# Performance work log

Hardware: AMD Instinct MI355X
Metric: run time of the kernel (lower is better)

## Reference

```python
import jax, jax.numpy as jnp
import numpy as np
import math

B, N, C_IN = 16, 4096, 1024
D, M, K, H = 64, 16, 64, 4  # projected dim, n prototypes, topk, heads


def setup_inputs() -> dict:
    key = jax.random.key(0)
    ks = jax.random.split(key, 8)
    return {
        "image_features": jax.random.normal(ks[0], (B, N, C_IN), jnp.float32),
        "W_down": jax.random.normal(ks[1], (C_IN, D), jnp.float32) * 0.02,
        "b_down": jnp.zeros((D,), jnp.float32),
        "W_up": jax.random.normal(ks[2], (D, C_IN), jnp.float32) * 0.02,
        "b_up": jnp.zeros((C_IN,), jnp.float32),
        "m_queries": jax.random.normal(ks[3], (1, M, D), jnp.float32),
        "ln_w": jnp.ones((D,), jnp.float32),
        "ln_b": jnp.zeros((D,), jnp.float32),
        "in_proj_w": jax.random.normal(ks[4], (3 * D, D), jnp.float32) * 0.05,
        "in_proj_b": jnp.zeros((3 * D,), jnp.float32),
        "out_proj_w": jax.random.normal(ks[5], (D, D), jnp.float32) * 0.05,
        "out_proj_b": jnp.zeros((D,), jnp.float32),
        "gamma": jnp.asarray(0.1, jnp.float32),
    }


@jax.custom_vjp
def ste_topk_mask(logits):
    # TopkSTE.forward: one-hot mask of top-k along dim 1
    _, idx = jax.lax.top_k(logits, K)
    oh = jnp.zeros_like(logits).at[jnp.arange(logits.shape[0])[:, None], idx].set(1.0)
    return oh


def _ste_fwd(logits):
    return ste_topk_mask(logits), logits


def _ste_bwd(logits, g):
    # TopkSTE.backward: grad_output * softmax(logits)
    return (g * jax.nn.softmax(logits, axis=1),)


ste_topk_mask.defvjp(_ste_fwd, _ste_bwd)


def _layernorm(x, w, b, eps=1e-5):
    mu = x.mean(-1, keepdims=True)
    var = ((x - mu) ** 2).mean(-1, keepdims=True)
    return (x - mu) * jax.lax.rsqrt(var + eps) * w + b


def _mha(x, in_w, in_b, out_w, out_b):
    # nn.MultiheadAttention self-attention, batch_first; x: [B,S,D]
    b, s, d = x.shape
    dh = d // H
    qkv = x @ in_w.T + in_b  # [B,S,3D]
    q, k, v = jnp.split(qkv, 3, axis=-1)
    split = lambda t: t.reshape(b, s, H, dh).transpose(0, 2, 1, 3)  # [B,H,S,dh]
    q, k, v = split(q), split(k), split(v)
    scores = jnp.einsum('bhqd,bhkd->bhqk', q, k) * (1.0 / math.sqrt(dh))
    attn = jax.nn.softmax(scores, axis=-1)
    o = jnp.einsum('bhqk,bhkd->bhqd', attn, v)
    o = o.transpose(0, 2, 1, 3).reshape(b, s, d)
    return o @ out_w.T + out_b


def reference(image_features, W_down, b_down, W_up, b_up, m_queries,
              ln_w, ln_b, in_proj_w, in_proj_b, out_proj_w, out_proj_b, gamma):
    identity = image_features
    act = jax.nn.gelu(image_features @ W_down + b_down)  # [B,N,D]; dropout = eval no-op

    # cosine similarity against prototypes -> max over prototypes
    nf = act / (jnp.linalg.norm(act, axis=-1, keepdims=True) + 1e-12)
    q0 = m_queries[0]
    nq = q0 / (jnp.linalg.norm(q0, axis=-1, keepdims=True) + 1e-12)
    scores = jnp.einsum('bnd,md->bnm', nf, nq).max(-1)  # [B,N]

    _ = ste_topk_mask(scores)  # mask only used to derive indices in original
    # torch mask.nonzero yields top-k indices in ascending order
    idx = jnp.sort(jax.lax.top_k(scores, K)[1], axis=1)  # [B,K]

    sparse = jnp.take_along_axis(act, idx[:, :, None], axis=1)  # [B,K,D]
    queries = jnp.broadcast_to(m_queries, (act.shape[0], M, D))
    seq = jnp.concatenate([queries, sparse], axis=1)  # [B,M+K,D]
    attn_out = _mha(_layernorm(seq, ln_w, ln_b), in_proj_w, in_proj_b, out_proj_w, out_proj_b)

    # scatter enhanced sparse tokens back, up-project, gamma-scaled residual
    enhanced_sparse = attn_out[:, M:, :]
    b_ix = jnp.arange(act.shape[0])[:, None]
    enhanced = act.at[b_ix, idx].set(enhanced_sparse)
    return identity + gamma * (enhanced @ W_up + b_up)
```

## Files before the change

kernel.cpp:

```cpp
#include <hip/hip_runtime.h>
#include <stdint.h>

typedef unsigned short u16;
typedef __bf16 bf16x8 __attribute__((ext_vector_type(8)));
typedef float f32x4 __attribute__((ext_vector_type(4)));

__device__ __forceinline__ u16 f2bf(float f) {
  union { float f; uint32_t u; } v; v.f = f;
  return (u16)((v.u + 0x7FFFu + ((v.u >> 16) & 1u)) >> 16);
}
__device__ __forceinline__ float bf2f(u16 u) {
  union { uint32_t u; float f; } v; v.u = ((uint32_t)u) << 16;
  return v.f;
}
__device__ __forceinline__ float gelu_tanh(float x) {
  float t = tanhf(0.7978845608028654f * (x + 0.044715f * x * x * x));
  return 0.5f * x * (1.0f + t);
}

__global__ __launch_bounds__(256) void k0_prep(const float* __restrict__ Wd,
                                               const float* __restrict__ Wu,
                                               const float* __restrict__ mq,
                                               u16* __restrict__ WdT, u16* __restrict__ WuT,
                                               float* __restrict__ nq) {
  int b = blockIdx.x, t = threadIdx.x;
  if (b < 256) {
    int e = b * 256 + t;
    int n = e >> 10, k = e & 1023;
    WdT[e] = f2bf(Wd[k * 64 + n]);
    int n2 = e >> 6, k2 = e & 63;
    WuT[e] = f2bf(Wu[k2 * 1024 + n2]);
  } else {
    if (t < 16) {
      float ss = 0.f;
      for (int c = 0; c < 64; c++) { float v = mq[t * 64 + c]; ss += v * v; }
      float inv = 1.0f / (sqrtf(ss) + 1e-12f);
      for (int c = 0; c < 64; c++) nq[t * 64 + c] = mq[t * 64 + c] * inv;
    }
  }
}

__global__ __launch_bounds__(256) void k1_gemm_down(const float* __restrict__ feat,
                                                    const u16* __restrict__ WdT,
                                                    const float* __restrict__ b_down,
                                                    const float* __restrict__ nq_g,
                                                    float* __restrict__ act,
                                                    float* __restrict__ scores) {
  __shared__ __align__(16) u16 Asm[64 * 72];
  __shared__ __align__(16) u16 Bsm[64 * 72];
  __shared__ float acts[64 * 65];
  __shared__ float nqs[16 * 64];
  int t = threadIdx.x;
  int lane = t & 63, w = t >> 6;
  int l15 = lane & 15, q = lane >> 4;
  long r0 = (long)blockIdx.x * 64;

  for (int i = t; i < 1024; i += 256) nqs[i] = nq_g[i];

  f32x4 acc[4] = {};
  int rloc = t >> 4;
  int col4 = (t & 15) * 4;
  int nB = t >> 2;
  int cB = t & 3;

  for (int kt = 0; kt < 16; kt++) {
    int k0 = kt * 64;
    __syncthreads();
    for (int p = 0; p < 4; p++) {
      int row = p * 16 + rloc;
      const float4 v = *(const float4*)&feat[(r0 + row) * 1024 + k0 + col4];
      ushort4 u; u.x = f2bf(v.x); u.y = f2bf(v.y); u.z = f2bf(v.z); u.w = f2bf(v.w);
      *(ushort4*)&Asm[row * 72 + col4] = u;
    }
    for (int h = 0; h < 2; h++) {
      int c = cB + h * 4;
      *(uint4*)&Bsm[nB * 72 + c * 8] = *(const uint4*)&WdT[nB * 1024 + k0 + c * 8];
    }
    __syncthreads();
    for (int ks = 0; ks < 2; ks++) {
      bf16x8 a = *(bf16x8*)&Asm[(w * 16 + l15) * 72 + ks * 32 + q * 8];
#pragma unroll
      for (int tn = 0; tn < 4; tn++) {
        bf16x8 bb = *(bf16x8*)&Bsm[(tn * 16 + l15) * 72 + ks * 32 + q * 8];
        acc[tn] = __builtin_amdgcn_mfma_f32_16x16x32_bf16(a, bb, acc[tn], 0, 0, 0);
      }
    }
  }
#pragma unroll
  for (int tn = 0; tn < 4; tn++) {
    int col = tn * 16 + l15;
    float bd = b_down[col];
#pragma unroll
    for (int j = 0; j < 4; j++) {
      int row = w * 16 + q * 4 + j;
      float g = gelu_tanh(acc[tn][j] + bd);
      act[(r0 + row) * 64 + col] = g;
      acts[row * 65 + col] = g;
    }
  }
  __syncthreads();
  {
    int r = t >> 2, p = t & 3;
    float ss = 0.f;
    float dots[16];
#pragma unroll
    for (int m = 0; m < 16; m++) dots[m] = 0.f;
    for (int i = 0; i < 16; i++) {
      int c = p * 16 + i;
      float v = acts[r * 65 + c];
      ss += v * v;
#pragma unroll
      for (int m = 0; m < 16; m++) dots[m] += v * nqs[m * 64 + c];
    }
    ss += __shfl_xor(ss, 1); ss += __shfl_xor(ss, 2);
#pragma unroll
    for (int m = 0; m < 16; m++) {
      dots[m] += __shfl_xor(dots[m], 1);
      dots[m] += __shfl_xor(dots[m], 2);
    }
    if (p == 0) {
      float inv = 1.0f / (sqrtf(ss) + 1e-12f);
      float best = -INFINITY;
#pragma unroll
      for (int m = 0; m < 16; m++) best = fmaxf(best, dots[m] * inv);
      scores[r0 + r] = best;
    }
  }
}

__global__ __launch_bounds__(256) void k2_topk(const float* __restrict__ scores,
                                               int* __restrict__ idx_out) {
  __shared__ float s[4096];
  __shared__ float wv[4];
  __shared__ int wi[4];
  __shared__ int list[64];
  __shared__ int slist[64];
  int b = blockIdx.x, t = threadIdx.x;
  for (int i = t; i < 4096; i += 256) s[i] = scores[b * 4096 + i];
  __syncthreads();
  for (int sel = 0; sel < 64; sel++) {
    float bv = -INFINITY; int bi = 0x7fffffff;
    for (int i = t; i < 4096; i += 256) {
      float v = s[i];
      if (v > bv || (v == bv && i < bi)) { bv = v; bi = i; }
    }
    for (int m = 1; m < 64; m <<= 1) {
      float ov = __shfl_xor(bv, m); int oi = __shfl_xor(bi, m);
      if (ov > bv || (ov == bv && oi < bi)) { bv = ov; bi = oi; }
    }
    if ((t & 63) == 0) { wv[t >> 6] = bv; wi[t >> 6] = bi; }
    __syncthreads();
    if (t == 0) {
      float fv = wv[0]; int fi = wi[0];
      for (int u2 = 1; u2 < 4; u2++)
        if (wv[u2] > fv || (wv[u2] == fv && wi[u2] < fi)) { fv = wv[u2]; fi = wi[u2]; }
      list[sel] = fi;
      s[fi] = -INFINITY;
    }
    __syncthreads();
  }
  if (t < 64) {
    int v = list[t], rank = 0;
    for (int j = 0; j < 64; j++) rank += (list[j] < v);
    slist[rank] = v;
  }
  __syncthreads();
  if (t < 64) idx_out[b * 64 + t] = slist[t];
}

__global__ __launch_bounds__(256) void k3a_ln_qkv(const float* __restrict__ act,
                                                  const float* __restrict__ mq,
                                                  const int* __restrict__ idx,
                                                  const float* __restrict__ lnw,
                                                  const float* __restrict__ lnb,
                                                  const float* __restrict__ inw,
                                                  const float* __restrict__ inb,
                                                  float* __restrict__ qkv) {
  __shared__ float xs[80 * 65];
  __shared__ u16 wsm[192 * 66];
  __shared__ int ii[64];
  int b = blockIdx.x, t = threadIdx.x;
  if (t < 64) ii[t] = idx[b * 64 + t];
  for (int e = t; e < 192 * 32; e += 256) {
    int j = e >> 5, cp = e & 31;
    uint32_t pk = (uint32_t)f2bf(inw[j * 64 + cp * 2]) |
                  ((uint32_t)f2bf(inw[j * 64 + cp * 2 + 1]) << 16);
    *(uint32_t*)&wsm[j * 66 + cp * 2] = pk;
  }
  __syncthreads();
  for (int e = t; e < 80 * 64; e += 256) {
    int r = e >> 6, c = e & 63;
    xs[r * 65 + c] = (r < 16) ? mq[r * 64 + c]
                              : act[((long)b * 4096 + ii[r - 16]) * 64 + c];
  }
  __syncthreads();
  if (t < 80) {
    float mu = 0.f;
    for (int c = 0; c < 64; c++) mu += xs[t * 65 + c];
    mu *= (1.0f / 64.0f);
    float var = 0.f;
    for (int c = 0; c < 64; c++) { float d = xs[t * 65 + c] - mu; var += d * d; }
    var *= (1.0f / 64.0f);
    float rs = 1.0f / sqrtf(var + 1e-5f);
    for (int c = 0; c < 64; c++)
      xs[t * 65 + c] = (xs[t * 65 + c] - mu) * rs * lnw[c] + lnb[c];
  }
  __syncthreads();
  for (int e = t; e < 80 * 192; e += 256) {
    int i = e / 192, j = e % 192;
    float s = inb[j];
    for (int d = 0; d < 64; d++) s += xs[i * 65 + d] * bf2f(wsm[j * 66 + d]);
    qkv[((long)b * 80 + i) * 192 + j] = s;
  }
}

__global__ __launch_bounds__(256) void k3b_attn(const float* __restrict__ qkv,
                                                float* __restrict__ attn_o) {
  __shared__ float qs[80 * 17], kk[80 * 17], vs[80 * 17];
  __shared__ float ps[80 * 81];
  int blk = blockIdx.x; int b = blk >> 2, h = blk & 3;
  int t = threadIdx.x;
  for (int e = t; e < 80 * 16; e += 256) {
    int i = e >> 4, d = e & 15;
    const float* base = &qkv[((long)b * 80 + i) * 192 + h * 16 + d];
    qs[i * 17 + d] = base[0];
    kk[i * 17 + d] = base[64];
    vs[i * 17 + d] = base[128];
  }
  __syncthreads();
  for (int e = t; e < 80 * 80; e += 256) {
    int i = e / 80, j = e % 80;
    float s = 0.f;
#pragma unroll
    for (int d = 0; d < 16; d++) s += qs[i * 17 + d] * kk[j * 17 + d];
    ps[i * 81 + j] = s * 0.25f;
  }
  __syncthreads();
  if (t < 80) {
    float mx = -INFINITY;
    for (int j = 0; j < 80; j++) mx = fmaxf(mx, ps[t * 81 + j]);
    float sum = 0.f;
    for (int j = 0; j < 80; j++) { float e2 = expf(ps[t * 81 + j] - mx); ps[t * 81 + j] = e2; sum += e2; }
    float inv = 1.0f / sum;
    for (int j = 0; j < 80; j++) ps[t * 81 + j] *= inv;
  }
  __syncthreads();
  for (int e = t; e < 80 * 16; e += 256) {
    int i = e >> 4, d = e & 15;
    float s = 0.f;
    for (int j = 0; j < 80; j++) s += ps[i * 81 + j] * vs[j * 17 + d];
    attn_o[((long)b * 80 + i) * 64 + h * 16 + d] = s;
  }
}

__global__ __launch_bounds__(256) void k3c_outproj(const float* __restrict__ attn_o,
                                                   const float* __restrict__ ow,
                                                   const float* __restrict__ ob,
                                                   const int* __restrict__ idx,
                                                   float* __restrict__ act) {
  __shared__ float os[64 * 64];
  __shared__ float wsm[64 * 65];
  __shared__ int ii[64];
  int b = blockIdx.x, t = threadIdx.x;
  if (t < 64) ii[t] = idx[b * 64 + t];
  for (int e = t; e < 4096; e += 256) {
    int r = e >> 6, c = e & 63;
    os[e] = attn_o[((long)b * 80 + 16 + r) * 64 + c];
    wsm[r * 65 + c] = ow[e];
  }
  __syncthreads();
  for (int e = t; e < 4096; e += 256) {
    int r = e >> 6, j = e & 63;
    float s = ob[j];
    for (int d = 0; d < 64; d++) s += os[r * 64 + d] * wsm[j * 65 + d];
    act[((long)b * 4096 + ii[r]) * 64 + j] = s;
  }
}

__global__ __launch_bounds__(256) void k4_gemm_up(const float* __restrict__ act,
                                                  const u16* __restrict__ WuT,
                                                  const float* __restrict__ identity,
                                                  const float* __restrict__ b_up,
                                                  const float* __restrict__ gamma,
                                                  float* __restrict__ out) {
  __shared__ __align__(16) u16 Asm[64 * 72];
  __shared__ __align__(16) u16 Bsm[256 * 72];
  int t = threadIdx.x;
  int lane = t & 63, w = t >> 6;
  int l15 = lane & 15, q = lane >> 4;
  int bx = blockIdx.x;
  long r0 = (long)(bx >> 2) * 64;
  int n0 = (bx & 3) * 256;

  {
    int col4 = (t & 15) * 4;
    int rloc = t >> 4;
    for (int p = 0; p < 4; p++) {
      int row = p * 16 + rloc;
      float4 v = *(const float4*)&act[(r0 + row) * 64 + col4];
      ushort4 u; u.x = f2bf(v.x); u.y = f2bf(v.y); u.z = f2bf(v.z); u.w = f2bf(v.w);
      *(ushort4*)&Asm[row * 72 + col4] = u;
    }
  }
  for (int c = 0; c < 8; c++)
    *(uint4*)&Bsm[t * 72 + c * 8] = *(const uint4*)&WuT[(n0 + t) * 64 + c * 8];
  __syncthreads();

  f32x4 acc[16] = {};
  for (int ks = 0; ks < 2; ks++) {
    bf16x8 a = *(bf16x8*)&Asm[(w * 16 + l15) * 72 + ks * 32 + q * 8];
#pragma unroll
    for (int tn = 0; tn < 16; tn++) {
      bf16x8 bb = *(bf16x8*)&Bsm[(tn * 16 + l15) * 72 + ks * 32 + q * 8];
      acc[tn] = __builtin_amdgcn_mfma_f32_16x16x32_bf16(a, bb, acc[tn], 0, 0, 0);
    }
  }
  float g = gamma[0];
#pragma unroll
  for (int tn = 0; tn < 16; tn++) {
    int col = n0 + tn * 16 + l15;
    float bu = b_up[col];
#pragma unroll
    for (int j = 0; j < 4; j++) {
      long row = r0 + w * 16 + q * 4 + j;
      long off = row * 1024 + col;
      out[off] = identity[off] + g * (acc[tn][j] + bu);
    }
  }
}

extern "C" void kernel_launch(void* const* d_in, const int* in_sizes, int n_in,
                              void* d_out, int out_size, void* d_ws, size_t ws_size,
                              hipStream_t stream) {
  const float* feat = (const float*)d_in[0];
  const float* Wd   = (const float*)d_in[1];
  const float* bd   = (const float*)d_in[2];
  const float* Wu   = (const float*)d_in[3];
  const float* bu   = (const float*)d_in[4];
  const float* mq   = (const float*)d_in[5];
  const float* lnw  = (const float*)d_in[6];
  const float* lnb  = (const float*)d_in[7];
  const float* inw  = (const float*)d_in[8];
  const float* inb  = (const float*)d_in[9];
  const float* ow   = (const float*)d_in[10];
  const float* ob   = (const float*)d_in[11];
  const float* gm   = (const float*)d_in[12];
  float* out = (float*)d_out;
  char* ws = (char*)d_ws;

  float* act    = (float*)(ws + 0);
  float* scores = (float*)(ws + 16777216);
  u16*   WdT    = (u16*)  (ws + 17039360);
  u16*   WuT    = (u16*)  (ws + 17170432);
  float* nq     = (float*)(ws + 17301504);
  int*   idx    = (int*)  (ws + 17305600);
  float* qkv    = (float*)(ws + 17309696);
  float* ao     = (float*)(ws + 18292736);

  hipLaunchKernelGGL(k0_prep,     dim3(257),  dim3(256), 0, stream, Wd, Wu, mq, WdT, WuT, nq);
  hipLaunchKernelGGL(k1_gemm_down,dim3(1024), dim3(256), 0, stream, feat, WdT, bd, nq, act, scores);
  hipLaunchKernelGGL(k2_topk,     dim3(16),   dim3(256), 0, stream, scores, idx);
  hipLaunchKernelGGL(k3a_ln_qkv,  dim3(16),   dim3(256), 0, stream, act, mq, idx, lnw, lnb, inw, inb, qkv);
  hipLaunchKernelGGL(k3b_attn,    dim3(64),   dim3(256), 0, stream, qkv, ao);
  hipLaunchKernelGGL(k3c_outproj, dim3(16),   dim3(256), 0, stream, ao, ow, ob, idx, act);
  hipLaunchKernelGGL(k4_gemm_up,  dim3(4096), dim3(256), 0, stream, act, WuT, feat, bu, gm, out);
}
```

Measured before the change: 822.3 us.

## Prefetch down-GEMM tiles, MFMA for QKV/outproj, vectorize up-GEMM epilogue via LDS

The down-projection GEMM now prefetches the next K tile from global memory into registers while MFMAs run on the current shared-memory tile. The QKV projection and out-projection move from scalar FP32 dot loops to bf16 MFMA tiles, and LayerNorm uses two threads per row with single-pass sums. The up-projection epilogue stages accumulators through LDS so identity reads and output writes become coalesced float4 accesses. These changes add bf16 rounding in the small projections, a single-pass variance formula, and more register pressure.

```diff
diff --git a/kernel.cpp b/kernel.cpp
--- a/kernel.cpp
+++ b/kernel.cpp
@@ -63,20 +63,36 @@
   int nB = t >> 2;
   int cB = t & 3;
 
+  float4 aReg[4];
+  uint4 bReg[2];
+#pragma unroll
+  for (int p = 0; p < 4; p++)
+    aReg[p] = *(const float4*)&feat[(r0 + p * 16 + rloc) * 1024 + col4];
+#pragma unroll
+  for (int h = 0; h < 2; h++)
+    bReg[h] = *(const uint4*)&WdT[nB * 1024 + (cB + h * 4) * 8];
+
   for (int kt = 0; kt < 16; kt++) {
-    int k0 = kt * 64;
-    __syncthreads();
+#pragma unroll
     for (int p = 0; p < 4; p++) {
-      int row = p * 16 + rloc;
-      const float4 v = *(const float4*)&feat[(r0 + row) * 1024 + k0 + col4];
-      ushort4 u; u.x = f2bf(v.x); u.y = f2bf(v.y); u.z = f2bf(v.z); u.w = f2bf(v.w);
-      *(ushort4*)&Asm[row * 72 + col4] = u;
-    }
-    for (int h = 0; h < 2; h++) {
-      int c = cB + h * 4;
-      *(uint4*)&Bsm[nB * 72 + c * 8] = *(const uint4*)&WdT[nB * 1024 + k0 + c * 8];
-    }
-    __syncthreads();
+      ushort4 u; u.x = f2bf(aReg[p].x); u.y = f2bf(aReg[p].y);
+      u.z = f2bf(aReg[p].z); u.w = f2bf(aReg[p].w);
+      *(ushort4*)&Asm[(p * 16 + rloc) * 72 + col4] = u;
+    }
+#pragma unroll
+    for (int h = 0; h < 2; h++)
+      *(uint4*)&Bsm[nB * 72 + (cB + h * 4) * 8] = bReg[h];
+    __syncthreads();
+    if (kt < 15) {
+      int k0 = (kt + 1) * 64;
+#pragma unroll
+      for (int p = 0; p < 4; p++)
+        aReg[p] = *(const float4*)&feat[(r0 + p * 16 + rloc) * 1024 + k0 + col4];
+#pragma unroll
+      for (int h = 0; h < 2; h++)
+        bReg[h] = *(const uint4*)&WdT[nB * 1024 + k0 + (cB + h * 4) * 8];
+    }
+#pragma unroll
     for (int ks = 0; ks < 2; ks++) {
       bf16x8 a = *(bf16x8*)&Asm[(w * 16 + l15) * 72 + ks * 32 + q * 8];
 #pragma unroll
@@ -85,6 +101,7 @@
         acc[tn] = __builtin_amdgcn_mfma_f32_16x16x32_bf16(a, bb, acc[tn], 0, 0, 0);
       }
     }
+    __syncthreads();
   }
 #pragma unroll
   for (int tn = 0; tn < 4; tn++) {
@@ -177,41 +194,65 @@
                                                   const float* __restrict__ inb,
                                                   float* __restrict__ qkv) {
   __shared__ float xs[80 * 65];
-  __shared__ u16 wsm[192 * 66];
+  __shared__ __align__(16) u16 xsb[80 * 72];
+  __shared__ __align__(16) u16 wb[192 * 72];
   __shared__ int ii[64];
   int b = blockIdx.x, t = threadIdx.x;
   if (t < 64) ii[t] = idx[b * 64 + t];
-  for (int e = t; e < 192 * 32; e += 256) {
-    int j = e >> 5, cp = e & 31;
-    uint32_t pk = (uint32_t)f2bf(inw[j * 64 + cp * 2]) |
-                  ((uint32_t)f2bf(inw[j * 64 + cp * 2 + 1]) << 16);
-    *(uint32_t*)&wsm[j * 66 + cp * 2] = pk;
+  for (int e = t; e < 192 * 64; e += 256) {
+    int j = e >> 6, d = e & 63;
+    wb[j * 72 + d] = f2bf(inw[e]);
   }
   __syncthreads();
   for (int e = t; e < 80 * 64; e += 256) {
     int r = e >> 6, c = e & 63;
-    xs[r * 65 + c] = (r < 16) ? mq[r * 64 + c]
+    xs[r * 65 + c] = (r < 16) ? mq[e]
                               : act[((long)b * 4096 + ii[r - 16]) * 64 + c];
   }
   __syncthreads();
-  if (t < 80) {
-    float mu = 0.f;
-    for (int c = 0; c < 64; c++) mu += xs[t * 65 + c];
-    mu *= (1.0f / 64.0f);
-    float var = 0.f;
-    for (int c = 0; c < 64; c++) { float d = xs[t * 65 + c] - mu; var += d * d; }
-    var *= (1.0f / 64.0f);
+  if (t < 160) {
+    int r = t >> 1, p = t & 1;
+    float s1 = 0.f, s2 = 0.f;
+    for (int c = p * 32; c < p * 32 + 32; c++) {
+      float v = xs[r * 65 + c]; s1 += v; s2 += v * v;
+    }
+    s1 += __shfl_xor(s1, 1); s2 += __shfl_xor(s2, 1);
+    float mu = s1 * (1.0f / 64.0f);
+    float var = s2 * (1.0f / 64.0f) - mu * mu;
     float rs = 1.0f / sqrtf(var + 1e-5f);
-    for (int c = 0; c < 64; c++)
-      xs[t * 65 + c] = (xs[t * 65 + c] - mu) * rs * lnw[c] + lnb[c];
-  }
-  __syncthreads();
-  for (int e = t; e < 80 * 192; e += 256) {
-    int i = e / 192, j = e % 192;
-    float s = inb[j];
-    for (int d = 0; d < 64; d++) s += xs[i * 65 + d] * bf2f(wsm[j * 66 + d]);
-    qkv[((long)b * 80 + i) * 192 + j] = s;
-  }
+    for (int c = p * 32; c < p * 32 + 32; c++) {
+      float v = (xs[r * 65 + c] - mu) * rs * lnw[c] + lnb[c];
+      xsb[r * 72 + c] = f2bf(v);
+    }
+  }
+  __syncthreads();
+  int lane = t & 63, w = t >> 6, l15 = lane & 15, q = lane >> 4;
+  f32x4 acc[15] = {};
+#pragma unroll
+  for (int m = 0; m < 5; m++) {
+    bf16x8 a0 = *(bf16x8*)&xsb[(m * 16 + l15) * 72 + q * 8];
+    bf16x8 a1 = *(bf16x8*)&xsb[(m * 16 + l15) * 72 + 32 + q * 8];
+#pragma unroll
+    for (int nn = 0; nn < 3; nn++) {
+      int n = w * 3 + nn;
+      bf16x8 b0 = *(bf16x8*)&wb[(n * 16 + l15) * 72 + q * 8];
+      bf16x8 b1 = *(bf16x8*)&wb[(n * 16 + l15) * 72 + 32 + q * 8];
+      acc[m * 3 + nn] = __builtin_amdgcn_mfma_f32_16x16x32_bf16(a0, b0, acc[m * 3 + nn], 0, 0, 0);
+      acc[m * 3 + nn] = __builtin_amdgcn_mfma_f32_16x16x32_bf16(a1, b1, acc[m * 3 + nn], 0, 0, 0);
+    }
+  }
+#pragma unroll
+  for (int m = 0; m < 5; m++)
+#pragma unroll
+    for (int nn = 0; nn < 3; nn++) {
+      int j = (w * 3 + nn) * 16 + l15;
+      float bias = inb[j];
+#pragma unroll
+      for (int jj = 0; jj < 4; jj++) {
+        int i = m * 16 + q * 4 + jj;
+        qkv[((long)b * 80 + i) * 192 + j] = acc[m * 3 + nn][jj] + bias;
+      }
+    }
 }
 
 __global__ __launch_bounds__(256) void k3b_attn(const float* __restrict__ qkv,
@@ -258,23 +299,37 @@
                                                    const float* __restrict__ ob,
                                                    const int* __restrict__ idx,
                                                    float* __restrict__ act) {
-  __shared__ float os[64 * 64];
-  __shared__ float wsm[64 * 65];
+  __shared__ __align__(16) u16 osb[64 * 72];
+  __shared__ __align__(16) u16 wbb[64 * 72];
   __shared__ int ii[64];
   int b = blockIdx.x, t = threadIdx.x;
   if (t < 64) ii[t] = idx[b * 64 + t];
   for (int e = t; e < 4096; e += 256) {
     int r = e >> 6, c = e & 63;
-    os[e] = attn_o[((long)b * 80 + 16 + r) * 64 + c];
-    wsm[r * 65 + c] = ow[e];
-  }
-  __syncthreads();
-  for (int e = t; e < 4096; e += 256) {
-    int r = e >> 6, j = e & 63;
-    float s = ob[j];
-    for (int d = 0; d < 64; d++) s += os[r * 64 + d] * wsm[j * 65 + d];
-    act[((long)b * 4096 + ii[r]) * 64 + j] = s;
-  }
+    osb[r * 72 + c] = f2bf(attn_o[((long)b * 80 + 16 + r) * 64 + c]);
+    wbb[r * 72 + c] = f2bf(ow[e]);
+  }
+  __syncthreads();
+  int lane = t & 63, w = t >> 6, l15 = lane & 15, q = lane >> 4;
+  f32x4 acc[4] = {};
+  bf16x8 b0 = *(bf16x8*)&wbb[(w * 16 + l15) * 72 + q * 8];
+  bf16x8 b1 = *(bf16x8*)&wbb[(w * 16 + l15) * 72 + 32 + q * 8];
+#pragma unroll
+  for (int m = 0; m < 4; m++) {
+    bf16x8 a0 = *(bf16x8*)&osb[(m * 16 + l15) * 72 + q * 8];
+    bf16x8 a1 = *(bf16x8*)&osb[(m * 16 + l15) * 72 + 32 + q * 8];
+    acc[m] = __builtin_amdgcn_mfma_f32_16x16x32_bf16(a0, b0, acc[m], 0, 0, 0);
+    acc[m] = __builtin_amdgcn_mfma_f32_16x16x32_bf16(a1, b1, acc[m], 0, 0, 0);
+  }
+  int j = w * 16 + l15;
+  float bias = ob[j];
+#pragma unroll
+  for (int m = 0; m < 4; m++)
+#pragma unroll
+    for (int jj = 0; jj < 4; jj++) {
+      int r = m * 16 + q * 4 + jj;
+      act[((long)b * 4096 + ii[r]) * 64 + j] = acc[m][jj] + bias;
+    }
 }
 
 __global__ __launch_bounds__(256) void k4_gemm_up(const float* __restrict__ act,
@@ -285,6 +340,7 @@
                                                   float* __restrict__ out) {
   __shared__ __align__(16) u16 Asm[64 * 72];
   __shared__ __align__(16) u16 Bsm[256 * 72];
+  float* Csm = (float*)Bsm;
   int t = threadIdx.x;
   int lane = t & 63, w = t >> 6;
   int l15 = lane & 15, q = lane >> 4;
@@ -307,6 +363,7 @@
   __syncthreads();
 
   f32x4 acc[16] = {};
+#pragma unroll
   for (int ks = 0; ks < 2; ks++) {
     bf16x8 a = *(bf16x8*)&Asm[(w * 16 + l15) * 72 + ks * 32 + q * 8];
 #pragma unroll
@@ -316,15 +373,33 @@
     }
   }
   float g = gamma[0];
-#pragma unroll
-  for (int tn = 0; tn < 16; tn++) {
-    int col = n0 + tn * 16 + l15;
-    float bu = b_up[col];
-#pragma unroll
-    for (int j = 0; j < 4; j++) {
-      long row = r0 + w * 16 + q * 4 + j;
-      long off = row * 1024 + col;
-      out[off] = identity[off] + g * (acc[tn][j] + bu);
+  int rdrow = t >> 4;
+  int rdcol4 = (t & 15) * 4;
+#pragma unroll
+  for (int c = 0; c < 4; c++) {
+    __syncthreads();
+#pragma unroll
+    for (int u2 = 0; u2 < 4; u2++) {
+      int tn = c * 4 + u2;
+      int lc = u2 * 16 + l15;
+      float bias = b_up[n0 + c * 64 + lc];
+#pragma unroll
+      for (int jj = 0; jj < 4; jj++) {
+        int row = w * 16 + q * 4 + jj;
+        Csm[row * 68 + lc] = acc[tn][jj] + bias;
+      }
+    }
+    __syncthreads();
+#pragma unroll
+    for (int p = 0; p < 4; p++) {
+      int row = p * 16 + rdrow;
+      long off = (r0 + row) * 1024 + n0 + c * 64 + rdcol4;
+      float4 cv = *(float4*)&Csm[row * 68 + rdcol4];
+      float4 iv = *(const float4*)&identity[off];
+      float4 ov;
+      ov.x = iv.x + g * cv.x; ov.y = iv.y + g * cv.y;
+      ov.z = iv.z + g * cv.z; ov.w = iv.w + g * cv.w;
+      *(float4*)&out[off] = ov;
     }
   }
 }
```

Result: faster. 746.4 us (-9.2%).
